# Kernel tuning notes

Hardware: AMD Instinct MI355X
Metric: run time of the kernel (lower is better)

## Reference

```python
import jax, jax.numpy as jnp
import numpy as np

D_MODEL = 1024
N_HEADS = 16
D_K = D_MODEL // N_HEADS
SCALE = 1.0 / np.sqrt(D_K).astype(np.float32)
NEG = -1000000000.0


def setup_inputs() -> dict:
    key = jax.random.key(0)
    ks = jax.random.split(key, 5)
    B, S = 2, 2048
    query = jax.random.normal(ks[0], (B, S, D_MODEL), dtype=jnp.float32)
    k_in = jax.random.normal(ks[1], (B, S, D_MODEL), dtype=jnp.float32)
    v_in = jax.random.normal(ks[2], (B, S, D_MODEL), dtype=jnp.float32)
    # causal mask, broadcast over batch and heads; 0 entries get -1e9
    mask = jnp.tril(jnp.ones((S, S), dtype=jnp.int32))[None, None, :, :]
    w_qkv = jax.random.normal(ks[3], (D_MODEL, 3 * D_MODEL), dtype=jnp.float32) * (1.0 / np.sqrt(D_MODEL))
    w_o = jax.random.normal(ks[4], (D_MODEL, D_MODEL), dtype=jnp.float32) * (1.0 / np.sqrt(D_MODEL))
    return {"query": query, "key": k_in, "value": v_in, "mask": mask, "w_qkv": w_qkv, "w_o": w_o}


def reference(query, key, value, mask, w_qkv, w_o):
    # NOTE: original module ignores `key`/`value`; q,k,v all come from `query`.
    B, S, _ = query.shape
    qkv = query @ w_qkv                       # [B,S,3D]
    q, k, v = jnp.split(qkv, 3, axis=-1)
    def heads(x):
        return x.reshape(B, S, N_HEADS, D_K).transpose(0, 2, 1, 3)  # [B,H,S,dk]
    Q, K, V = heads(q), heads(k), heads(v)
    scores = jnp.einsum('bhqd,bhkd->bhqk', Q, K) * SCALE            # [B,H,S,S]
    scores = jnp.where(mask == 0, NEG, scores)
    attn = jax.nn.softmax(scores, axis=-1)
    # Dropout(0.1) treated as eval-mode identity for a deterministic reference.
    context = jnp.einsum('bhqk,bhkd->bhqd', attn, V)                # [B,H,S,dk]
    context = context.transpose(0, 2, 1, 3).reshape(B, S, D_MODEL)
    return context @ w_o
```

## Files before the change

### kernel.cpp

```cpp
#include <hip/hip_runtime.h>
#include <stdint.h>


typedef __attribute__((ext_vector_type(8))) short bf16x8;
typedef __attribute__((ext_vector_type(4))) float f32x4;

#define LOG2E 1.44269504088896340736f
#define QSCALE (0.125f * LOG2E)

__device__ __forceinline__ unsigned short f2b(float f) {
  union { float f; unsigned int i; } x; x.f = f;
  unsigned int i = x.i;
  return (unsigned short)((i + 0x7FFFu + ((i >> 16) & 1u)) >> 16);
}

__device__ __forceinline__ void async16(const void* g, void* l) {
  __builtin_amdgcn_global_load_lds(
      (__attribute__((address_space(1))) void*)g,
      (__attribute__((address_space(3))) void*)l, 16, 0, 0);
}

__device__ __forceinline__ f32x4 mfma16(bf16x8 a, bf16x8 b, f32x4 c) {
  return __builtin_amdgcn_mfma_f32_16x16x32_bf16(a, b, c, 0, 0, 0);
}

__device__ __forceinline__ unsigned int fbits(float f) {
  union { float f; unsigned int i; } x; x.f = f;
  return x.i;
}

__global__ __launch_bounds__(256) void prep(
    const float* __restrict__ X, const float* __restrict__ Wqkv,
    const float* __restrict__ Wo, unsigned short* __restrict__ Xb,
    unsigned short* __restrict__ WqkvT, unsigned short* __restrict__ WoT) {
  __shared__ __align__(16) unsigned short Lt[64 * 64];
  const int bx = blockIdx.x;
  const int t = threadIdx.x;
  if (bx < 2048) {
    const size_t i = ((size_t)bx * 256 + t) * 8;
    float4 a = *(const float4*)(X + i);
    float4 b = *(const float4*)(X + i + 4);
    unsigned short e[8];
    e[0] = f2b(a.x); e[1] = f2b(a.y); e[2] = f2b(a.z); e[3] = f2b(a.w);
    e[4] = f2b(b.x); e[5] = f2b(b.y); e[6] = f2b(b.z); e[7] = f2b(b.w);
    *(uint4*)(Xb + i) = *(const uint4*)e;
    return;
  }
  const bool is_qkv = (bx < 2816);
  const int bid = is_qkv ? bx - 2048 : bx - 2816;
  const float* src = is_qkv ? Wqkv : Wo;
  unsigned short* dst = is_qkv ? WqkvT : WoT;
  const int Ccols = is_qkv ? 3072 : 1024;
  const int r0 = (bid & 15) * 64, c0 = (bid >> 4) * 64;
  const float s = (is_qkv && c0 < 1024) ? QSCALE : 1.0f;
#pragma unroll
  for (int it = 0; it < 4; ++it) {
    int c = it * 256 + t;
    int sr = c >> 4, co = (c & 15) * 4;
    float4 v = *(const float4*)(src + (size_t)(r0 + sr) * Ccols + c0 + co);
    Lt[(co + 0) * 64 + sr] = f2b(v.x * s);
    Lt[(co + 1) * 64 + sr] = f2b(v.y * s);
    Lt[(co + 2) * 64 + sr] = f2b(v.z * s);
    Lt[(co + 3) * 64 + sr] = f2b(v.w * s);
  }
  __syncthreads();
#pragma unroll
  for (int it = 0; it < 2; ++it) {
    int c = it * 256 + t;
    int dr = c >> 3, so = (c & 7) * 8;
    *(uint4*)(dst + (size_t)(c0 + dr) * 1024 + r0 + so) =
        *(const uint4*)(Lt + dr * 64 + so);
  }
}

__global__ __launch_bounds__(256) void gemm_qkv(
    const unsigned short* __restrict__ A, const unsigned short* __restrict__ Bt,
    unsigned short* __restrict__ C, unsigned short* __restrict__ Vt) {
  constexpr int K = 1024, N = 3072;
  __shared__ __align__(16) unsigned short Sm[16896];
  unsigned short* As = Sm;
  unsigned short* Bs = Sm + 8192;
  unsigned short* Lt = Sm;

  const int t = threadIdx.x;
  const int w = t >> 6, l = t & 63;
  const int m0 = blockIdx.y * 128, n0 = blockIdx.x * 128;
  const int wm = (w >> 1) * 64, wn = (w & 1) * 64;
  const int lrow = l & 15, lq = l >> 4;

  f32x4 acc[4][4] = {};

  for (int k0 = 0; k0 < K; k0 += 64) {
    __syncthreads();
#pragma unroll
    for (int r = 0; r < 4; ++r) {
      const int c = r * 256 + t;
      const int row = c >> 3;
      const int so = ((c & 7) ^ (row & 7)) * 8;
      async16(A + (size_t)(m0 + row) * K + k0 + so,
              As + (size_t)(r * 256 + t) * 8);
      async16(Bt + (size_t)(n0 + row) * K + k0 + so,
              Bs + (size_t)(r * 256 + t) * 8);
    }
    asm volatile("s_waitcnt vmcnt(0)" ::: "memory");
    __syncthreads();

#pragma unroll
    for (int kh = 0; kh < 2; ++kh) {
      bf16x8 af[4], bf[4];
      const int phys = ((kh * 4 + lq) ^ (lrow & 7)) * 8;
#pragma unroll
      for (int i = 0; i < 4; ++i)
        af[i] = *(const bf16x8*)(As + (wm + i * 16 + lrow) * 64 + phys);
#pragma unroll
      for (int j = 0; j < 4; ++j)
        bf[j] = *(const bf16x8*)(Bs + (wn + j * 16 + lrow) * 64 + phys);
#pragma unroll
      for (int i = 0; i < 4; ++i)
#pragma unroll
        for (int j = 0; j < 4; ++j)
          acc[i][j] = mfma16(af[i], bf[j], acc[i][j]);
    }
  }

  if (n0 < 2048) {
#pragma unroll
    for (int i = 0; i < 4; ++i)
#pragma unroll
      for (int j = 0; j < 4; ++j)
#pragma unroll
        for (int r = 0; r < 4; ++r) {
          int gr = m0 + wm + i * 16 + lq * 4 + r;
          int gc = n0 + wn + j * 16 + lrow;
          C[(size_t)gr * N + gc] = f2b(acc[i][j][r]);
        }
  } else {
    __syncthreads();
#pragma unroll
    for (int i = 0; i < 4; ++i)
#pragma unroll
      for (int j = 0; j < 4; ++j) {
        int col_loc = wn + j * 16 + lrow;
        int row_loc = wm + i * 16 + lq * 4;
        uint2 pk;
        pk.x = (unsigned int)f2b(acc[i][j][0]) |
               ((unsigned int)f2b(acc[i][j][1]) << 16);
        pk.y = (unsigned int)f2b(acc[i][j][2]) |
               ((unsigned int)f2b(acc[i][j][3]) << 16);
        *(uint2*)(Lt + col_loc * 132 + row_loc) = pk;
      }
    __syncthreads();
    const int b = m0 >> 11, s0 = m0 & 2047;
    const int vb0 = n0 - 2048;
#pragma unroll
    for (int rnd = 0; rnd < 8; ++rnd) {
      int vrow = rnd * 16 + (t >> 4);
      int sloc = (t & 15) * 8;
      int vcol = vb0 + vrow;
      int bh = b * 16 + (vcol >> 6);
      int d = vcol & 63;
      *(uint4*)(Vt + ((size_t)bh * 64 + d) * 2048 + s0 + sloc) =
          *(const uint4*)(Lt + vrow * 132 + sloc);
    }
  }
}

__global__ __launch_bounds__(256) void gemm_o(
    const unsigned short* __restrict__ A, const unsigned short* __restrict__ Bt,
    float* __restrict__ C, int M, int N, int K) {
  __shared__ __align__(16) unsigned short As[128 * 64];
  __shared__ __align__(16) unsigned short Bs[128 * 64];
  const int t = threadIdx.x;
  const int w = t >> 6, l = t & 63;
  const int m0 = blockIdx.y * 128, n0 = blockIdx.x * 128;
  const int wm = (w >> 1) * 64, wn = (w & 1) * 64;
  const int lrow = l & 15, lq = l >> 4;

  f32x4 acc[4][4] = {};

  for (int k0 = 0; k0 < K; k0 += 64) {
    __syncthreads();
#pragma unroll
    for (int r = 0; r < 4; ++r) {
      const int c = r * 256 + t;
      const int row = c >> 3;
      const int so = ((c & 7) ^ (row & 7)) * 8;
      async16(A + (size_t)(m0 + row) * K + k0 + so,
              As + (size_t)(r * 256 + t) * 8);
      async16(Bt + (size_t)(n0 + row) * K + k0 + so,
              Bs + (size_t)(r * 256 + t) * 8);
    }
    asm volatile("s_waitcnt vmcnt(0)" ::: "memory");
    __syncthreads();

#pragma unroll
    for (int kh = 0; kh < 2; ++kh) {
      bf16x8 af[4], bf[4];
      const int phys = ((kh * 4 + lq) ^ (lrow & 7)) * 8;
#pragma unroll
      for (int i = 0; i < 4; ++i)
        af[i] = *(const bf16x8*)(As + (wm + i * 16 + lrow) * 64 + phys);
#pragma unroll
      for (int j = 0; j < 4; ++j)
        bf[j] = *(const bf16x8*)(Bs + (wn + j * 16 + lrow) * 64 + phys);
#pragma unroll
      for (int i = 0; i < 4; ++i)
#pragma unroll
        for (int j = 0; j < 4; ++j)
          acc[i][j] = mfma16(af[i], bf[j], acc[i][j]);
    }
  }

#pragma unroll
  for (int i = 0; i < 4; ++i)
#pragma unroll
    for (int j = 0; j < 4; ++j)
#pragma unroll
      for (int r = 0; r < 4; ++r) {
        int gr = m0 + wm + i * 16 + lq * 4 + r;
        int gc = n0 + wn + j * 16 + lrow;
        C[(size_t)gr * N + gc] = acc[i][j][r];
      }
}

__global__ __launch_bounds__(512, 4) void attn_fwd(
    const unsigned short* __restrict__ qkv,
    const unsigned short* __restrict__ Vt,
    unsigned short* __restrict__ ctx) {
  __shared__ __align__(16) unsigned short Ks[2][64 * 64];
  __shared__ __align__(16) unsigned short Vs[2][64 * 64];
  __shared__ __align__(16) unsigned short Ps[8][16 * 72];

  const int bh = blockIdx.x;
  const int ti = 31 - blockIdx.y;
  const int b = bh >> 4, h = bh & 15;
  const int t = threadIdx.x;
  const int g = t >> 8;
  const int tl = t & 255;
  const int w = tl >> 6;
  const int gw = t >> 6;
  const int l = t & 63;
  const int lm = l & 15, lq = l >> 4;
  const int sw = lm & 7;
  const int c0 = (lq ^ sw) * 8;
  const int c1 = ((lq + 4) ^ sw) * 8;

  const unsigned short* Qp = qkv + (size_t)(b * 2048) * 3072 + h * 64;
  const unsigned short* Kp = qkv + (size_t)(b * 2048) * 3072 + 1024 + h * 64;
  const unsigned short* Vb = Vt + (size_t)bh * 64 * 2048;

  const int qrow = ti * 64 + w * 16 + lm;
  bf16x8 qf0 = *(const bf16x8*)(Qp + (size_t)qrow * 3072 + lq * 8);
  bf16x8 qf1 = *(const bf16x8*)(Qp + (size_t)qrow * 3072 + 32 + lq * 8);

  const int srow = tl >> 3, scp = tl & 7;
  const int sso = (scp ^ (srow & 7)) * 8;
  const unsigned short* kp0 = Kp + (size_t)(g * 64 + srow) * 3072 + sso;
  const unsigned short* kp1 = kp0 + (size_t)32 * 3072;
  const unsigned short* vp0 = Vb + (size_t)srow * 2048 + g * 64 + sso;
  const unsigned short* vp1 = vp0 + (size_t)32 * 2048;
  unsigned short* kd0 = Ks[g] + (size_t)(w * 64) * 8;
  unsigned short* kd1 = Ks[g] + (size_t)(256 + w * 64) * 8;
  unsigned short* vd0 = Vs[g] + (size_t)(w * 64) * 8;
  unsigned short* vd1 = Vs[g] + (size_t)(256 + w * 64) * 8;

  f32x4 oacc[4] = {};
  float lsum = 0.f;

  const int nsup = (ti >> 1) + 1;

  for (int jj = 0; jj < nsup; ++jj) {
    const int kt = 2 * jj + g;
    const bool have = (kt <= ti);
    __syncthreads();
    if (have) {
      async16(kp0, kd0);
      async16(vp0, vd0);
      async16(kp1, kd1);
      async16(vp1, vd1);
    }
    kp0 += 128 * 3072; kp1 += 128 * 3072;
    vp0 += 128; vp1 += 128;
    asm volatile("s_waitcnt vmcnt(0)" ::: "memory");
    __syncthreads();
    if (!have) continue;

    const unsigned short* Kc = Ks[g];
    const unsigned short* Vc = Vs[g];

    bf16x8 vf[8];
#pragma unroll
    for (int nt = 0; nt < 4; ++nt) {
      const unsigned short* vr = Vc + (nt * 16 + lm) * 64;
      vf[nt] = *(const bf16x8*)(vr + c0);
      vf[4 + nt] = *(const bf16x8*)(vr + c1);
    }

    f32x4 sacc[4] = {};
    __builtin_amdgcn_s_setprio(1);
#pragma unroll
    for (int mt = 0; mt < 4; ++mt) {
      const unsigned short* kr = Kc + (mt * 16 + lm) * 64;
      bf16x8 bk0 = *(const bf16x8*)(kr + c0);
      bf16x8 bk1 = *(const bf16x8*)(kr + c1);
      sacc[mt] = mfma16(bk0, qf0, sacc[mt]);
      sacc[mt] = mfma16(bk1, qf1, sacc[mt]);
    }
    __builtin_amdgcn_s_setprio(0);

    const bool diag = (kt == ti);
    const int qloc = w * 16 + lm;
#pragma unroll
    for (int mt = 0; mt < 4; ++mt) {
      float p0 = __builtin_amdgcn_exp2f(sacc[mt][0]);
      float p1 = __builtin_amdgcn_exp2f(sacc[mt][1]);
      float p2 = __builtin_amdgcn_exp2f(sacc[mt][2]);
      float p3 = __builtin_amdgcn_exp2f(sacc[mt][3]);
      if (diag) {
        const int kvb = mt * 16 + lq * 4;
        if (kvb + 0 > qloc) p0 = 0.f;
        if (kvb + 1 > qloc) p1 = 0.f;
        if (kvb + 2 > qloc) p2 = 0.f;
        if (kvb + 3 > qloc) p3 = 0.f;
      }
      lsum += (p0 + p1) + (p2 + p3);
      uint2 pk;
      pk.x = (fbits(p1) & 0xFFFF0000u) | (fbits(p0) >> 16);
      pk.y = (fbits(p3) & 0xFFFF0000u) | (fbits(p2) >> 16);
      *(uint2*)(&Ps[gw][lm * 72 + mt * 16 + lq * 4]) = pk;
    }
    asm volatile("s_waitcnt lgkmcnt(0)" ::: "memory");

    __builtin_amdgcn_s_setprio(1);
#pragma unroll
    for (int ks = 0; ks < 2; ++ks) {
      bf16x8 pa = *(const bf16x8*)(&Ps[gw][lm * 72 + ks * 32 + lq * 8]);
#pragma unroll
      for (int nt = 0; nt < 4; ++nt)
        oacc[nt] = mfma16(pa, vf[ks * 4 + nt], oacc[nt]);
    }
    __builtin_amdgcn_s_setprio(0);
  }

  lsum += __shfl_xor(lsum, 16, 64);
  lsum += __shfl_xor(lsum, 32, 64);

  __syncthreads();
  float* fbuf = (float*)Ks;
  float* lbuf = (float*)Ps;
  if (g == 1) {
#pragma unroll
    for (int nt = 0; nt < 4; ++nt)
#pragma unroll
      for (int r = 0; r < 4; ++r)
        fbuf[(w * 16 + lq * 4 + r) * 64 + nt * 16 + lm] = oacc[nt][r];
    if (l < 16) lbuf[w * 16 + lm] = lsum;
  }
  __syncthreads();
  if (g == 0) {
    const float ltot = lsum + lbuf[w * 16 + lm];
    float rinv[4];
#pragma unroll
    for (int r = 0; r < 4; ++r)
      rinv[r] = 1.f / __shfl(ltot, lq * 4 + r, 64);
#pragma unroll
    for (int nt = 0; nt < 4; ++nt)
#pragma unroll
      for (int r = 0; r < 4; ++r) {
        float v = oacc[nt][r] +
                  fbuf[(w * 16 + lq * 4 + r) * 64 + nt * 16 + lm];
        size_t tok = (size_t)b * 2048 + ti * 64 + w * 16 + lq * 4 + r;
        ctx[tok * 1024 + h * 64 + nt * 16 + lm] = f2b(v * rinv[r]);
      }
  }
}

extern "C" void kernel_launch(void* const* d_in, const int* in_sizes, int n_in,
                              void* d_out, int out_size, void* d_ws,
                              size_t ws_size, hipStream_t stream) {
  const float* query = (const float*)d_in[0];
  const float* w_qkv = (const float*)d_in[4];
  const float* w_o = (const float*)d_in[5];
  float* out = (float*)d_out;

  unsigned short* ws = (unsigned short*)d_ws;
  unsigned short* wqkvT = ws;
  unsigned short* woT = wqkvT + (size_t)3072 * 1024;
  unsigned short* Xb = woT + (size_t)1024 * 1024;
  unsigned short* qkv = Xb + (size_t)4096 * 1024;
  unsigned short* Vt = qkv + (size_t)4096 * 3072;
  unsigned short* ctx = Xb;

  prep<<<dim3(3072), 256, 0, stream>>>(query, w_qkv, w_o, Xb, wqkvT, woT);
  gemm_qkv<<<dim3(24, 32), 256, 0, stream>>>(Xb, wqkvT, qkv, Vt);
  attn_fwd<<<dim3(32, 32), 512, 0, stream>>>(qkv, Vt, ctx);
  gemm_o<<<dim3(8, 32), 256, 0, stream>>>(ctx, woT, out, 4096, 1024, 1024);
}
```

Before: 203.6 us.

## Double-buffer K/V tiles in attention and swizzle GEMM block order

The attention kernel now gives each K/V tile group two LDS buffers. The next tile's async global-to-LDS loads are issued before the current tile is computed, with one barrier per iteration, so load latency can overlap the MFMA and softmax work. Both GEMM kernels remap block indices with a grouped swizzle, so concurrently running blocks share A/B tiles in cache. The extra buffers roughly double the attention kernel's LDS use, which lowers achievable occupancy. No explicit vmcnt wait remains before reading the prefetched buffer, so correctness depends on compiler-inserted waits.

```diff
diff --git a/kernel.cpp b/kernel.cpp
--- a/kernel.cpp
+++ b/kernel.cpp
@@ -84,7 +84,9 @@
 
   const int t = threadIdx.x;
   const int w = t >> 6, l = t & 63;
-  const int m0 = blockIdx.y * 128, n0 = blockIdx.x * 128;
+  const int flat = blockIdx.x + 24 * blockIdx.y;
+  const int swz = (flat & 7) * 96 + (flat >> 3);
+  const int m0 = (swz / 24) * 128, n0 = (swz % 24) * 128;
   const int wm = (w >> 1) * 64, wn = (w & 1) * 64;
   const int lrow = l & 15, lq = l >> 4;
 
@@ -172,7 +174,9 @@
   __shared__ __align__(16) unsigned short Bs[128 * 64];
   const int t = threadIdx.x;
   const int w = t >> 6, l = t & 63;
-  const int m0 = blockIdx.y * 128, n0 = blockIdx.x * 128;
+  const int flat = blockIdx.x + 8 * blockIdx.y;
+  const int swz = (flat & 7) * 32 + (flat >> 3);
+  const int m0 = (swz >> 3) * 128, n0 = (swz & 7) * 128;
   const int wm = (w >> 1) * 64, wn = (w & 1) * 64;
   const int lrow = l & 15, lq = l >> 4;
 
@@ -227,8 +231,8 @@
     const unsigned short* __restrict__ qkv,
     const unsigned short* __restrict__ Vt,
     unsigned short* __restrict__ ctx) {
-  __shared__ __align__(16) unsigned short Ks[2][64 * 64];
-  __shared__ __align__(16) unsigned short Vs[2][64 * 64];
+  __shared__ __align__(16) unsigned short Ks[2][2][64 * 64];
+  __shared__ __align__(16) unsigned short Vs[2][2][64 * 64];
   __shared__ __align__(16) unsigned short Ps[8][16 * 72];
 
   const int bh = blockIdx.x;
@@ -259,93 +263,104 @@
   const unsigned short* kp1 = kp0 + (size_t)32 * 3072;
   const unsigned short* vp0 = Vb + (size_t)srow * 2048 + g * 64 + sso;
   const unsigned short* vp1 = vp0 + (size_t)32 * 2048;
-  unsigned short* kd0 = Ks[g] + (size_t)(w * 64) * 8;
-  unsigned short* kd1 = Ks[g] + (size_t)(256 + w * 64) * 8;
-  unsigned short* vd0 = Vs[g] + (size_t)(w * 64) * 8;
-  unsigned short* vd1 = Vs[g] + (size_t)(256 + w * 64) * 8;
+  unsigned short* kd0 = Ks[g][0] + (size_t)(w * 64) * 8;
+  unsigned short* kd1 = Ks[g][0] + (size_t)(256 + w * 64) * 8;
+  unsigned short* vd0 = Vs[g][0] + (size_t)(w * 64) * 8;
+  unsigned short* vd1 = Vs[g][0] + (size_t)(256 + w * 64) * 8;
 
   f32x4 oacc[4] = {};
   float lsum = 0.f;
 
   const int nsup = (ti >> 1) + 1;
 
-  for (int jj = 0; jj < nsup; ++jj) {
-    const int kt = 2 * jj + g;
-    const bool have = (kt <= ti);
-    __syncthreads();
-    if (have) {
-      async16(kp0, kd0);
-      async16(vp0, vd0);
-      async16(kp1, kd1);
-      async16(vp1, vd1);
-    }
+  if (g <= ti) {
+    async16(kp0, kd0);
+    async16(vp0, vd0);
+    async16(kp1, kd1);
+    async16(vp1, vd1);
     kp0 += 128 * 3072; kp1 += 128 * 3072;
     vp0 += 128; vp1 += 128;
-    asm volatile("s_waitcnt vmcnt(0)" ::: "memory");
-    __syncthreads();
-    if (!have) continue;
-
-    const unsigned short* Kc = Ks[g];
-    const unsigned short* Vc = Vs[g];
-
-    bf16x8 vf[8];
-#pragma unroll
-    for (int nt = 0; nt < 4; ++nt) {
-      const unsigned short* vr = Vc + (nt * 16 + lm) * 64;
-      vf[nt] = *(const bf16x8*)(vr + c0);
-      vf[4 + nt] = *(const bf16x8*)(vr + c1);
-    }
-
-    f32x4 sacc[4] = {};
-    __builtin_amdgcn_s_setprio(1);
-#pragma unroll
-    for (int mt = 0; mt < 4; ++mt) {
-      const unsigned short* kr = Kc + (mt * 16 + lm) * 64;
-      bf16x8 bk0 = *(const bf16x8*)(kr + c0);
-      bf16x8 bk1 = *(const bf16x8*)(kr + c1);
-      sacc[mt] = mfma16(bk0, qf0, sacc[mt]);
-      sacc[mt] = mfma16(bk1, qf1, sacc[mt]);
-    }
-    __builtin_amdgcn_s_setprio(0);
-
-    const bool diag = (kt == ti);
-    const int qloc = w * 16 + lm;
-#pragma unroll
-    for (int mt = 0; mt < 4; ++mt) {
-      float p0 = __builtin_amdgcn_exp2f(sacc[mt][0]);
-      float p1 = __builtin_amdgcn_exp2f(sacc[mt][1]);
-      float p2 = __builtin_amdgcn_exp2f(sacc[mt][2]);
-      float p3 = __builtin_amdgcn_exp2f(sacc[mt][3]);
-      if (diag) {
-        const int kvb = mt * 16 + lq * 4;
-        if (kvb + 0 > qloc) p0 = 0.f;
-        if (kvb + 1 > qloc) p1 = 0.f;
-        if (kvb + 2 > qloc) p2 = 0.f;
-        if (kvb + 3 > qloc) p3 = 0.f;
-      }
-      lsum += (p0 + p1) + (p2 + p3);
-      uint2 pk;
-      pk.x = (fbits(p1) & 0xFFFF0000u) | (fbits(p0) >> 16);
-      pk.y = (fbits(p3) & 0xFFFF0000u) | (fbits(p2) >> 16);
-      *(uint2*)(&Ps[gw][lm * 72 + mt * 16 + lq * 4]) = pk;
-    }
-    asm volatile("s_waitcnt lgkmcnt(0)" ::: "memory");
-
-    __builtin_amdgcn_s_setprio(1);
-#pragma unroll
-    for (int ks = 0; ks < 2; ++ks) {
-      bf16x8 pa = *(const bf16x8*)(&Ps[gw][lm * 72 + ks * 32 + lq * 8]);
-#pragma unroll
-      for (int nt = 0; nt < 4; ++nt)
-        oacc[nt] = mfma16(pa, vf[ks * 4 + nt], oacc[nt]);
-    }
-    __builtin_amdgcn_s_setprio(0);
+  }
+  __syncthreads();
+
+  for (int jj = 0; jj < nsup; ++jj) {
+    const int p = jj & 1;
+    const int kt = 2 * jj + g;
+
+    if (kt + 2 <= ti) {
+      const int po = (p ^ 1) * 4096;
+      async16(kp0, kd0 + po);
+      async16(vp0, vd0 + po);
+      async16(kp1, kd1 + po);
+      async16(vp1, vd1 + po);
+      kp0 += 128 * 3072; kp1 += 128 * 3072;
+      vp0 += 128; vp1 += 128;
+    }
+
+    if (kt <= ti) {
+      const unsigned short* Kc = Ks[g][p];
+      const unsigned short* Vc = Vs[g][p];
+
+      bf16x8 vf[8];
+#pragma unroll
+      for (int nt = 0; nt < 4; ++nt) {
+        const unsigned short* vr = Vc + (nt * 16 + lm) * 64;
+        vf[nt] = *(const bf16x8*)(vr + c0);
+        vf[4 + nt] = *(const bf16x8*)(vr + c1);
+      }
+
+      f32x4 sacc[4] = {};
+      __builtin_amdgcn_s_setprio(1);
+#pragma unroll
+      for (int mt = 0; mt < 4; ++mt) {
+        const unsigned short* kr = Kc + (mt * 16 + lm) * 64;
+        bf16x8 bk0 = *(const bf16x8*)(kr + c0);
+        bf16x8 bk1 = *(const bf16x8*)(kr + c1);
+        sacc[mt] = mfma16(bk0, qf0, sacc[mt]);
+        sacc[mt] = mfma16(bk1, qf1, sacc[mt]);
+      }
+      __builtin_amdgcn_s_setprio(0);
+
+      const bool diag = (kt == ti);
+      const int qloc = w * 16 + lm;
+#pragma unroll
+      for (int mt = 0; mt < 4; ++mt) {
+        float p0 = __builtin_amdgcn_exp2f(sacc[mt][0]);
+        float p1 = __builtin_amdgcn_exp2f(sacc[mt][1]);
+        float p2 = __builtin_amdgcn_exp2f(sacc[mt][2]);
+        float p3 = __builtin_amdgcn_exp2f(sacc[mt][3]);
+        if (diag) {
+          const int kvb = mt * 16 + lq * 4;
+          if (kvb + 0 > qloc) p0 = 0.f;
+          if (kvb + 1 > qloc) p1 = 0.f;
+          if (kvb + 2 > qloc) p2 = 0.f;
+          if (kvb + 3 > qloc) p3 = 0.f;
+        }
+        lsum += (p0 + p1) + (p2 + p3);
+        uint2 pk;
+        pk.x = (fbits(p1) & 0xFFFF0000u) | (fbits(p0) >> 16);
+        pk.y = (fbits(p3) & 0xFFFF0000u) | (fbits(p2) >> 16);
+        *(uint2*)(&Ps[gw][lm * 72 + mt * 16 + lq * 4]) = pk;
+      }
+      asm volatile("s_waitcnt lgkmcnt(0)" ::: "memory");
+
+      __builtin_amdgcn_s_setprio(1);
+#pragma unroll
+      for (int ks = 0; ks < 2; ++ks) {
+        bf16x8 pa = *(const bf16x8*)(&Ps[gw][lm * 72 + ks * 32 + lq * 8]);
+#pragma unroll
+        for (int nt = 0; nt < 4; ++nt)
+          oacc[nt] = mfma16(pa, vf[ks * 4 + nt], oacc[nt]);
+      }
+      __builtin_amdgcn_s_setprio(0);
+    }
+
+    __syncthreads();
   }
 
   lsum += __shfl_xor(lsum, 16, 64);
   lsum += __shfl_xor(lsum, 32, 64);
 
-  __syncthreads();
   float* fbuf = (float*)Ks;
   float* lbuf = (float*)Ps;
   if (g == 1) {
```

Result: slower. 211.3 us (+3.8%).
